# Kernel tuning notes

Hardware: AMD Instinct MI355X
Metric: run time of the kernel (lower is better)

The kernel has to match this reference:

```python
import jax, jax.numpy as jnp
import numpy as np

EPS = 1e-6
H = 12  # num_attention_heads

def _phi(x):
    # feature map used by fast-transformers LinearAttention: elu(x) + 1
    return jax.nn.elu(x) + 1.0

def setup_inputs() -> dict:
    key = jax.random.key(0)
    k1, k2, k3 = jax.random.split(key, 3)
    B, N, D = 32, 1024, 768
    x = jax.random.normal(k1, (B, N, D), dtype=jnp.float32)
    W_qkv = jax.random.normal(k2, (D, 3 * D), dtype=jnp.float32) * (D ** -0.5)
    W_out = jax.random.normal(k3, (D, D), dtype=jnp.float32) * (D ** -0.5)
    b_out = jnp.zeros((D,), dtype=jnp.float32)
    return {"x": x, "W_qkv": W_qkv, "W_out": W_out, "b_out": b_out}

def reference(x, W_qkv, W_out, b_out):
    B, N, D = x.shape
    d = D // H
    # F.pad(x, [0,0,0,1]): append one zero token along sequence
    x_ = jnp.pad(x, ((0, 0), (0, 1), (0, 0)))              # [B, N+1, D]
    qkv = x_ @ W_qkv                                        # [B, N+1, 3D]
    q, k, v = jnp.split(qkv, 3, axis=-1)
    q = q.reshape(B, N + 1, H, d)
    k = k.reshape(B, N + 1, H, d)
    v = v.reshape(B, N + 1, H, d)
    # non-causal linear attention (mask is all-ones -> no masking)
    q = _phi(q)
    k = _phi(k)
    kv = jnp.einsum('bshd,bshm->bhdm', k, v)                # [B, H, d, d]
    z = 1.0 / (jnp.einsum('blhd,bhd->blh', q, k.sum(axis=1)) + EPS)
    out = jnp.einsum('blhd,bhdm,blh->blhm', q, kv, z)       # [B, N+1, H, d]
    out = out.reshape(B, N + 1, D)
    out = out @ W_out + b_out                               # dropout = identity (eval)
    return out[:, :-1, :]                                   # drop padding token
```

## Files before the change

### kernel.cpp

```cpp
#include <hip/hip_runtime.h>
#include <hip/hip_bf16.h>


typedef __bf16 bf16x8 __attribute__((ext_vector_type(8)));
typedef float f32x4 __attribute__((ext_vector_type(4)));

__device__ __forceinline__ ushort f2bf(float f) {
  union { float f; unsigned u; } x; x.f = f;
  unsigned r = x.u + 0x7fffu + ((x.u >> 16) & 1u);
  return (ushort)(r >> 16);
}
__device__ __forceinline__ float bf2f(ushort h) {
  union { unsigned u; float f; } x; x.u = ((unsigned)h) << 16;
  return x.f;
}
__device__ __forceinline__ float bits2f(unsigned u) {
  union { unsigned u; float f; } x; x.u = u;
  return x.f;
}
__device__ __forceinline__ void gload_lds16(const void* g, void* lds) {
  __builtin_amdgcn_global_load_lds((const __attribute__((address_space(1))) void*)g,
                                   (__attribute__((address_space(3))) void*)lds, 16, 0, 0);
}

__global__ __launch_bounds__(256) void cvt_f32_bf16(const float* __restrict__ in,
                                                    ushort* __restrict__ out, int n4) {
  int i = blockIdx.x * 256 + threadIdx.x;
  if (i >= n4) return;
  float4 v = reinterpret_cast<const float4*>(in)[i];
  ushort4 o;
  o.x = f2bf(v.x); o.y = f2bf(v.y); o.z = f2bf(v.z); o.w = f2bf(v.w);
  reinterpret_cast<ushort4*>(out)[i] = o;
}

__global__ __launch_bounds__(256) void transpose_cvt(const float* __restrict__ src,
                                                     ushort* __restrict__ dst, int R, int C) {
  __shared__ float tile[32][33];
  int bc = blockIdx.x * 32, br = blockIdx.y * 32;
  int tx = threadIdx.x & 31, ty = threadIdx.x >> 5;
  #pragma unroll
  for (int i = 0; i < 32; i += 8)
    tile[ty + i][tx] = src[(size_t)(br + ty + i) * C + (bc + tx)];
  __syncthreads();
  #pragma unroll
  for (int i = 0; i < 32; i += 8)
    dst[(size_t)(bc + ty + i) * R + (br + tx)] = f2bf(tile[tx][ty + i]);
}

template <int MODE>
__global__ __launch_bounds__(512, 4) void gemm3b(const ushort* __restrict__ A,
                                                 const ushort* __restrict__ Bt,
                                                 void* __restrict__ C,
                                                 const float* __restrict__ bias,
                                                 int N, int K, int nbx, int cpx) {
  extern __shared__ ushort lds[];
  const int tid = threadIdx.x;
  const int lane = tid & 63;
  const int wid = tid >> 6;
  const int wm = wid >> 2, wn = wid & 3;
  const int laneR = lane & 15, laneS = lane >> 4;

  const int bid = blockIdx.x;
  const int lin = (bid & 7) * cpx + (bid >> 3);
  const int by = lin / nbx, bx = lin - by * nbx;
  const int m0 = by * 128, n0 = bx * 256;
  const int NT = K >> 5;

  const int sr = tid >> 2, ss = tid & 3;
  const int sslot = ss ^ ((sr >> 1) & 3);
  const ushort* Asrc = A + (size_t)(m0 + sr) * K + sslot * 8;
  const ushort* Bsrc = Bt + (size_t)(n0 + sr) * K + sslot * 8;
  const size_t rowstep128 = (size_t)128 * K;
  const int ldstA = tid * 8;
  const int ldstB = 4096 + tid * 8;

  const int sprime = laneS ^ ((laneR >> 1) & 3);
  const int aoff = (wm * 64 + laneR) * 32 + sprime * 8;
  const int boff = 4096 + (wn * 64 + laneR) * 32 + sprime * 8;

  f32x4 acc[4][4] = {};

  #define SBAR  __builtin_amdgcn_sched_barrier(0)
  #define STAGE_T(KT, DB)                                                         \
    { gload_lds16(Asrc + (KT) * 32, lds + (DB) + ldstA);                          \
      gload_lds16(Bsrc + (KT) * 32, lds + (DB) + ldstB);                          \
      gload_lds16(Bsrc + (KT) * 32 + rowstep128, lds + (DB) + ldstB + 4096); }

  STAGE_T(0, 0);
  STAGE_T(1, 12288);
  asm volatile("s_waitcnt vmcnt(3)" ::: "memory");
  SBAR;
  __builtin_amdgcn_s_barrier();
  SBAR;

  for (int t = 0; t < NT; ++t) {
    const ushort* cb = lds + (t % 3) * 12288;
    const int db2 = ((t + 2) % 3) * 12288;
    const int t2 = (t + 2 < NT) ? t + 2 : t;
    bf16x8 a[4], b[4];
    #pragma unroll
    for (int j = 0; j < 4; ++j) b[j] = *(const bf16x8*)(cb + boff + j * 512);
    #pragma unroll
    for (int i = 0; i < 4; ++i) a[i] = *(const bf16x8*)(cb + aoff + i * 512);
    STAGE_T(t2, db2);
    asm volatile("s_waitcnt vmcnt(3)" ::: "memory");
    SBAR;
    __builtin_amdgcn_s_barrier();
    SBAR;
    __builtin_amdgcn_s_setprio(1);
    #pragma unroll
    for (int i = 0; i < 4; ++i)
      #pragma unroll
      for (int j = 0; j < 4; ++j)
        acc[i][j] = __builtin_amdgcn_mfma_f32_16x16x32_bf16(a[i], b[j], acc[i][j], 0, 0, 0);
    __builtin_amdgcn_s_setprio(0);
    SBAR;
    __builtin_amdgcn_s_barrier();
    SBAR;
  }
  #undef STAGE_T
  asm volatile("s_waitcnt vmcnt(0)" ::: "memory");

  #pragma unroll
  for (int i = 0; i < 4; ++i) {
    const int grow0 = m0 + wm * 64 + i * 16 + (laneS << 2);
    #pragma unroll
    for (int j = 0; j < 4; ++j) {
      const int gcol = n0 + wn * 64 + j * 16 + laneR;
      #pragma unroll
      for (int r = 0; r < 4; ++r) {
        float v = acc[i][j][r];
        if (MODE == 0) {
          if (gcol < 1536) v = (v > 0.f) ? (v + 1.f) : __expf(v);
          reinterpret_cast<ushort*>(C)[(size_t)(grow0 + r) * N + gcol] = f2bf(v);
        } else {
          reinterpret_cast<float*>(C)[(size_t)(grow0 + r) * N + gcol] = v + bias[gcol];
        }
      }
    }
  }
}

__global__ __launch_bounds__(256) void kv_partial(const ushort* __restrict__ qkv,
                                                  float* __restrict__ kv_part,
                                                  float* __restrict__ ks_part) {
  const int blk = blockIdx.x;
  const int bh = blk >> 2, sp = blk & 3;
  const int b = bh / 12, h = bh % 12;
  const int tid = threadIdx.x;
  __shared__ float Ks[32 * 68];
  __shared__ float Vs[32 * 68];
  float acc[4][4] = {};
  float kacc[4] = {};
  const int dq0 = (tid & 15) * 4, mq0 = (tid >> 4) * 4;
  const int r = tid >> 3, o = (tid & 7) * 8;
  for (int st = 0; st < 256; st += 32) {
    const size_t rowbase = (size_t)(b * 1024 + sp * 256 + st + r) * 2304 + h * 64 + o;
    int4 kraw = *reinterpret_cast<const int4*>(qkv + rowbase + 768);
    int4 vraw = *reinterpret_cast<const int4*>(qkv + rowbase + 1536);
    float kf[8], vf[8];
    {
      const unsigned* kw = reinterpret_cast<const unsigned*>(&kraw);
      const unsigned* vw = reinterpret_cast<const unsigned*>(&vraw);
      #pragma unroll
      for (int w = 0; w < 4; ++w) {
        kf[2 * w]     = bits2f(kw[w] << 16);
        kf[2 * w + 1] = bits2f(kw[w] & 0xffff0000u);
        vf[2 * w]     = bits2f(vw[w] << 16);
        vf[2 * w + 1] = bits2f(vw[w] & 0xffff0000u);
      }
    }
    __syncthreads();
    #pragma unroll
    for (int w = 0; w < 8; ++w) {
      Ks[r * 68 + o + w] = kf[w];
      Vs[r * 68 + o + w] = vf[w];
    }
    __syncthreads();
    #pragma unroll 8
    for (int s = 0; s < 32; ++s) {
      f32x4 kk = *reinterpret_cast<const f32x4*>(&Ks[s * 68 + dq0]);
      f32x4 vv = *reinterpret_cast<const f32x4*>(&Vs[s * 68 + mq0]);
      #pragma unroll
      for (int jm = 0; jm < 4; ++jm)
        #pragma unroll
        for (int id = 0; id < 4; ++id)
          acc[jm][id] += vv[jm] * kk[id];
      if (mq0 == 0) {
        #pragma unroll
        for (int id = 0; id < 4; ++id) kacc[id] += kk[id];
      }
    }
  }
  float* kvp = kv_part + ((size_t)sp * 384 + bh) * 4096;
  #pragma unroll
  for (int jm = 0; jm < 4; ++jm)
    #pragma unroll
    for (int id = 0; id < 4; ++id)
      kvp[(mq0 + jm) * 64 + dq0 + id] = acc[jm][id];
  if (mq0 == 0) {
    #pragma unroll
    for (int id = 0; id < 4; ++id)
      ks_part[((size_t)sp * 384 + bh) * 64 + dq0 + id] = kacc[id];
  }
}

__global__ __launch_bounds__(256) void kv_reduce(const float* __restrict__ kv_part,
                                                 const float* __restrict__ ks_part,
                                                 ushort* __restrict__ kv_bf,
                                                 float* __restrict__ ksum) {
  int i = blockIdx.x * 256 + threadIdx.x;
  if (i < 384 * 4096) {
    float s = 0.f;
    #pragma unroll
    for (int p = 0; p < 4; ++p) s += kv_part[(size_t)p * (384 * 4096) + i];
    kv_bf[i] = f2bf(s);
  }
  if (i < 384 * 64) {
    float s = 1.0f;
    #pragma unroll
    for (int p = 0; p < 4; ++p) s += ks_part[(size_t)p * (384 * 64) + i];
    ksum[i] = s;
  }
}

__global__ __launch_bounds__(256) void attn_kernel(const ushort* __restrict__ qkv,
                                                   const ushort* __restrict__ kv_bf,
                                                   const float* __restrict__ ksum,
                                                   ushort* __restrict__ attn) {
  const int blk = blockIdx.x;
  const int bh = blk >> 3, tb = blk & 7;
  const int b = bh / 12, h = bh % 12;
  const int row0 = b * 1024 + tb * 128;
  __shared__ ushort Qs[128 * 64];
  __shared__ ushort KVs[64 * 64];
  __shared__ float zs[128];
  __shared__ float ks_lds[64];
  const int tid = threadIdx.x;
  const int lane = tid & 63, w = tid >> 6;
  #pragma unroll
  for (int j = 0; j < 4; ++j) {
    int c = j * 256 + tid;
    int qr = c >> 3, dsl = c & 7;
    int ssl = dsl ^ (qr & 7);
    gload_lds16(qkv + (size_t)(row0 + qr) * 2304 + h * 64 + ssl * 8, &Qs[c * 8]);
  }
  #pragma unroll
  for (int j = 0; j < 2; ++j) {
    int c = j * 256 + tid;
    int mr = c >> 3, dsl = c & 7;
    int ssl = dsl ^ (mr & 7);
    gload_lds16(kv_bf + (size_t)bh * 4096 + mr * 64 + ssl * 8, &KVs[c * 8]);
  }
  if (tid < 64) ks_lds[tid] = ksum[bh * 64 + tid];
  asm volatile("s_waitcnt vmcnt(0)" ::: "memory");
  __syncthreads();
  if (tid < 128) {
    float d = 0.f;
    const int tx7 = tid & 7;
    #pragma unroll
    for (int s = 0; s < 8; ++s) {
      int4 raw = *reinterpret_cast<const int4*>(&Qs[tid * 64 + ((s ^ tx7) << 3)]);
      const unsigned* wds = reinterpret_cast<const unsigned*>(&raw);
      #pragma unroll
      for (int w2 = 0; w2 < 4; ++w2) {
        d += bits2f(wds[w2] << 16) * ks_lds[s * 8 + 2 * w2];
        d += bits2f(wds[w2] & 0xffff0000u) * ks_lds[s * 8 + 2 * w2 + 1];
      }
    }
    zs[tid] = 1.f / (d + 1e-6f);
  }
  __syncthreads();
  f32x4 acc[2][4] = {};
  const int lr7 = (lane & 15) & 7;
  #pragma unroll
  for (int ks = 0; ks < 2; ++ks) {
    const int sxor = ((ks * 4 + (lane >> 4)) ^ lr7) << 3;
    bf16x8 a[2], bb[4];
    #pragma unroll
    for (int i = 0; i < 2; ++i)
      a[i] = *reinterpret_cast<const bf16x8*>(&Qs[(w * 32 + i * 16 + (lane & 15)) * 64 + sxor]);
    #pragma unroll
    for (int j = 0; j < 4; ++j)
      bb[j] = *reinterpret_cast<const bf16x8*>(&KVs[(j * 16 + (lane & 15)) * 64 + sxor]);
    #pragma unroll
    for (int i = 0; i < 2; ++i)
      #pragma unroll
      for (int j = 0; j < 4; ++j)
        acc[i][j] = __builtin_amdgcn_mfma_f32_16x16x32_bf16(a[i], bb[j], acc[i][j], 0, 0, 0);
  }
  #pragma unroll
  for (int i = 0; i < 2; ++i) {
    const int t0 = w * 32 + i * 16 + ((lane >> 4) << 2);
    #pragma unroll
    for (int j = 0; j < 4; ++j) {
      const int m = j * 16 + (lane & 15);
      #pragma unroll
      for (int r = 0; r < 4; ++r) {
        float v = acc[i][j][r] * zs[t0 + r];
        attn[(size_t)(row0 + t0 + r) * 768 + h * 64 + m] = f2bf(v);
      }
    }
  }
}

extern "C" void kernel_launch(void* const* d_in, const int* in_sizes, int n_in,
                              void* d_out, int out_size, void* d_ws, size_t ws_size,
                              hipStream_t stream) {
  (void)in_sizes; (void)n_in; (void)out_size; (void)ws_size;
  const float* x    = (const float*)d_in[0];
  const float* Wqkv = (const float*)d_in[1];
  const float* Wout = (const float*)d_in[2];
  const float* bout = (const float*)d_in[3];
  float* out = (float*)d_out;
  char* ws = (char*)d_ws;

  ushort* xbf    = (ushort*)(ws);
  ushort* wqkvT  = (ushort*)(ws + 50331648);
  ushort* woutT  = (ushort*)(ws + 53870592);
  ushort* qkv    = (ushort*)(ws + 55050240);
  float*  ksp    = (float*) (ws + 206045184);
  ushort* kvbf   = (ushort*)(ws + 206438400);
  float*  ksum   = (float*) (ws + 209584128);
  float*  kvpart = (float*)(ws);
  ushort* attn   = (ushort*)(ws);

  static const int LDS3 = 73728;
  hipFuncSetAttribute(reinterpret_cast<const void*>(&gemm3b<0>),
                      hipFuncAttributeMaxDynamicSharedMemorySize, LDS3);
  hipFuncSetAttribute(reinterpret_cast<const void*>(&gemm3b<1>),
                      hipFuncAttributeMaxDynamicSharedMemorySize, LDS3);

  cvt_f32_bf16<<<24576, 256, 0, stream>>>(x, xbf, 6291456);
  transpose_cvt<<<dim3(72, 24), 256, 0, stream>>>(Wqkv, wqkvT, 768, 2304);
  transpose_cvt<<<dim3(24, 24), 256, 0, stream>>>(Wout, woutT, 768, 768);
  gemm3b<0><<<2304, 512, LDS3, stream>>>(xbf, wqkvT, qkv, nullptr, 2304, 768, 9, 288);
  kv_partial<<<1536, 256, 0, stream>>>(qkv, kvpart, ksp);
  kv_reduce<<<6144, 256, 0, stream>>>(kvpart, ksp, kvbf, ksum);
  attn_kernel<<<3072, 256, 0, stream>>>(qkv, kvbf, ksum, attn);
  gemm3b<1><<<768, 512, LDS3, stream>>>(attn, woutT, out, bout, 768, 768, 3, 96);
}
```

Before: 290.4 us.

## Fuse fp32-to-bf16 conversion of x into the QKV GEMM prologue

```diff
diff --git a/kernel.cpp b/kernel.cpp
--- a/kernel.cpp
+++ b/kernel.cpp
@@ -4,6 +4,8 @@
 
 typedef __bf16 bf16x8 __attribute__((ext_vector_type(8)));
 typedef float f32x4 __attribute__((ext_vector_type(4)));
+
+#define SBAR  __builtin_amdgcn_sched_barrier(0)
 
 __device__ __forceinline__ ushort f2bf(float f) {
   union { float f; unsigned u; } x; x.f = f;
@@ -22,15 +24,23 @@
   __builtin_amdgcn_global_load_lds((const __attribute__((address_space(1))) void*)g,
                                    (__attribute__((address_space(3))) void*)lds, 16, 0, 0);
 }
-
-__global__ __launch_bounds__(256) void cvt_f32_bf16(const float* __restrict__ in,
-                                                    ushort* __restrict__ out, int n4) {
-  int i = blockIdx.x * 256 + threadIdx.x;
-  if (i >= n4) return;
-  float4 v = reinterpret_cast<const float4*>(in)[i];
-  ushort4 o;
-  o.x = f2bf(v.x); o.y = f2bf(v.y); o.z = f2bf(v.z); o.w = f2bf(v.w);
-  reinterpret_cast<ushort4*>(out)[i] = o;
+__device__ __forceinline__ void ds_write128(ushort* p, bf16x8 v) {
+  asm volatile("ds_write_b128 %0, %1"
+               :: "v"((__attribute__((address_space(3))) ushort*)p), "v"(v)
+               : "memory");
+}
+__device__ __forceinline__ f32x4 gloadf4(const float* p) {
+  f32x4 r;
+  asm volatile("global_load_dwordx4 %0, %1, off"
+               : "=v"(r)
+               : "v"(p));
+  return r;
+}
+__device__ __forceinline__ bf16x8 cvt8(f32x4 a, f32x4 b) {
+  bf16x8 v;
+  v[0] = (__bf16)a[0]; v[1] = (__bf16)a[1]; v[2] = (__bf16)a[2]; v[3] = (__bf16)a[3];
+  v[4] = (__bf16)b[0]; v[5] = (__bf16)b[1]; v[6] = (__bf16)b[2]; v[7] = (__bf16)b[3];
+  return v;
 }
 
 __global__ __launch_bounds__(256) void transpose_cvt(const float* __restrict__ src,
@@ -45,6 +55,115 @@
   #pragma unroll
   for (int i = 0; i < 32; i += 8)
     dst[(size_t)(bc + ty + i) * R + (br + tx)] = f2bf(tile[tx][ty + i]);
+}
+
+__global__ __launch_bounds__(512, 4) void gemm1f(const float* __restrict__ X,
+                                                 const ushort* __restrict__ Bt,
+                                                 ushort* __restrict__ C,
+                                                 int N, int K, int nbx, int cpx) {
+  extern __shared__ ushort lds[];
+  const int tid = threadIdx.x;
+  const int lane = tid & 63;
+  const int wid = tid >> 6;
+  const int wm = wid >> 2, wn = wid & 3;
+  const int laneR = lane & 15, laneS = lane >> 4;
+
+  const int bid = blockIdx.x;
+  const int lin = (bid & 7) * cpx + (bid >> 3);
+  const int by = lin / nbx, bx = lin - by * nbx;
+  const int m0 = by * 128, n0 = bx * 256;
+  const int NT = K >> 5;
+
+  const int sr = tid >> 2, ss = tid & 3;
+  const int sslot = ss ^ ((sr >> 1) & 3);
+  const float*  Axf  = X + (size_t)(m0 + sr) * K + sslot * 8;
+  const ushort* Bsrc = Bt + (size_t)(n0 + sr) * K + sslot * 8;
+  const size_t rowstep128 = (size_t)128 * K;
+  const int ldstA = tid * 8;
+  const int ldstB = 4096 + tid * 8;
+
+  const int sprime = laneS ^ ((laneR >> 1) & 3);
+  const int aoff = (wm * 64 + laneR) * 32 + sprime * 8;
+  const int boff = 4096 + (wn * 64 + laneR) * 32 + sprime * 8;
+
+  f32x4 acc[4][4] = {};
+  f32x4 rE0, rE1, rO0, rO1;
+
+  {
+    rE0 = gloadf4(Axf);      rE1 = gloadf4(Axf + 4);
+    rO0 = gloadf4(Axf + 32); rO1 = gloadf4(Axf + 36);
+    asm volatile("s_waitcnt vmcnt(0)" ::: "memory");
+    SBAR;
+    ds_write128(lds + ldstA, cvt8(rE0, rE1));
+    ds_write128(lds + 12288 + ldstA, cvt8(rO0, rO1));
+    gload_lds16(Bsrc,               lds + ldstB);
+    gload_lds16(Bsrc + rowstep128,  lds + ldstB + 4096);
+    gload_lds16(Bsrc + 32,              lds + 12288 + ldstB);
+    gload_lds16(Bsrc + 32 + rowstep128, lds + 12288 + ldstB + 4096);
+    rE0 = gloadf4(Axf + 64); rE1 = gloadf4(Axf + 68);
+    asm volatile("s_waitcnt vmcnt(0)" ::: "memory");
+    SBAR;
+    asm volatile("s_waitcnt lgkmcnt(0)" ::: "memory");
+    SBAR;
+    __builtin_amdgcn_s_barrier();
+    SBAR;
+  }
+
+  #define PHASE1F(T, WR0, WR1, IS0, IS1)                                          \
+  {                                                                               \
+    const int t_ = (T);                                                           \
+    const ushort* cb = lds + (t_ % 3) * 12288;                                    \
+    const int db2 = ((t_ + 2) % 3) * 12288;                                       \
+    const int t2 = (t_ + 2 < NT) ? t_ + 2 : t_;                                   \
+    const int t3 = (t_ + 3 < NT) ? t_ + 3 : t_;                                   \
+    bf16x8 a_[4], b_[4];                                                          \
+    _Pragma("unroll")                                                             \
+    for (int j = 0; j < 4; ++j) b_[j] = *(const bf16x8*)(cb + boff + j * 512);    \
+    _Pragma("unroll")                                                             \
+    for (int i = 0; i < 4; ++i) a_[i] = *(const bf16x8*)(cb + aoff + i * 512);    \
+    IS0 = gloadf4(Axf + t3 * 32); IS1 = gloadf4(Axf + t3 * 32 + 4);               \
+    gload_lds16(Bsrc + t2 * 32,              lds + db2 + ldstB);                  \
+    gload_lds16(Bsrc + t2 * 32 + rowstep128, lds + db2 + ldstB + 4096);           \
+    asm volatile("s_waitcnt vmcnt(4)" ::: "memory");                              \
+    SBAR;          \
+    ds_write128(lds + db2 + ldstA, cvt8(WR0, WR1));                               \
+    asm volatile("s_waitcnt lgkmcnt(0)" ::: "memory");                            \
+    SBAR;                                                                         \
+    __builtin_amdgcn_s_barrier();                                                 \
+    SBAR;                                                                         \
+    __builtin_amdgcn_s_setprio(1);                                                \
+    _Pragma("unroll")                                                             \
+    for (int i = 0; i < 4; ++i)                                                   \
+      _Pragma("unroll")                                                           \
+      for (int j = 0; j < 4; ++j)                                                 \
+        acc[i][j] = __builtin_amdgcn_mfma_f32_16x16x32_bf16(a_[i], b_[j], acc[i][j], 0, 0, 0); \
+    __builtin_amdgcn_s_setprio(0);                                                \
+    SBAR;                                                                         \
+    __builtin_amdgcn_s_barrier();                                                 \
+    SBAR;                                                                         \
+  }
+
+  for (int it = 0; it < NT; it += 2) {
+    PHASE1F(it,     rE0, rE1, rO0, rO1);
+    PHASE1F(it + 1, rO0, rO1, rE0, rE1);
+  }
+  #undef PHASE1F
+  asm volatile("s_waitcnt vmcnt(0)" ::: "memory");
+
+  #pragma unroll
+  for (int i = 0; i < 4; ++i) {
+    const int grow0 = m0 + wm * 64 + i * 16 + (laneS << 2);
+    #pragma unroll
+    for (int j = 0; j < 4; ++j) {
+      const int gcol = n0 + wn * 64 + j * 16 + laneR;
+      #pragma unroll
+      for (int r = 0; r < 4; ++r) {
+        float v = acc[i][j][r];
+        if (gcol < 1536) v = (v > 0.f) ? (v + 1.f) : __expf(v);
+        C[(size_t)(grow0 + r) * N + gcol] = f2bf(v);
+      }
+    }
+  }
 }
 
 template <int MODE>
@@ -80,7 +199,6 @@
 
   f32x4 acc[4][4] = {};
 
-  #define SBAR  __builtin_amdgcn_sched_barrier(0)
   #define STAGE_T(KT, DB)                                                         \
     { gload_lds16(Asrc + (KT) * 32, lds + (DB) + ldstA);                          \
       gload_lds16(Bsrc + (KT) * 32, lds + (DB) + ldstB);                          \
@@ -315,7 +433,6 @@
   float* out = (float*)d_out;
   char* ws = (char*)d_ws;
 
-  ushort* xbf    = (ushort*)(ws);
   ushort* wqkvT  = (ushort*)(ws + 50331648);
   ushort* woutT  = (ushort*)(ws + 53870592);
   ushort* qkv    = (ushort*)(ws + 55050240);
@@ -326,15 +443,14 @@
   ushort* attn   = (ushort*)(ws);
 
   static const int LDS3 = 73728;
-  hipFuncSetAttribute(reinterpret_cast<const void*>(&gemm3b<0>),
+  hipFuncSetAttribute(reinterpret_cast<const void*>(&gemm1f),
                       hipFuncAttributeMaxDynamicSharedMemorySize, LDS3);
   hipFuncSetAttribute(reinterpret_cast<const void*>(&gemm3b<1>),
                       hipFuncAttributeMaxDynamicSharedMemorySize, LDS3);
 
-  cvt_f32_bf16<<<24576, 256, 0, stream>>>(x, xbf, 6291456);
   transpose_cvt<<<dim3(72, 24), 256, 0, stream>>>(Wqkv, wqkvT, 768, 2304);
   transpose_cvt<<<dim3(24, 24), 256, 0, stream>>>(Wout, woutT, 768, 768);
-  gemm3b<0><<<2304, 512, LDS3, stream>>>(xbf, wqkvT, qkv, nullptr, 2304, 768, 9, 288);
+  gemm1f<<<2304, 512, LDS3, stream>>>(x, wqkvT, qkv, 2304, 768, 9, 288);
   kv_partial<<<1536, 256, 0, stream>>>(qkv, kvpart, ksp);
   kv_reduce<<<6144, 256, 0, stream>>>(kvpart, ksp, kvbf, ksum);
   attn_kernel<<<3072, 256, 0, stream>>>(qkv, kvbf, ksum, attn);
```

Result: slower. 345.2 us (+18.9%).

## Add 256x128-tile 4-wave QKV GEMM with fused elu+1 epilogue

Applied to the files above, without the earlier changes.

```diff
diff --git a/kernel.cpp b/kernel.cpp
--- a/kernel.cpp
+++ b/kernel.cpp
@@ -4,6 +4,8 @@
 
 typedef __bf16 bf16x8 __attribute__((ext_vector_type(8)));
 typedef float f32x4 __attribute__((ext_vector_type(4)));
+
+#define SBAR  __builtin_amdgcn_sched_barrier(0)
 
 __device__ __forceinline__ ushort f2bf(float f) {
   union { float f; unsigned u; } x; x.f = f;
@@ -45,6 +47,96 @@
   #pragma unroll
   for (int i = 0; i < 32; i += 8)
     dst[(size_t)(bc + ty + i) * R + (br + tx)] = f2bf(tile[tx][ty + i]);
+}
+
+__global__ __launch_bounds__(256, 2) void gemm1w(const ushort* __restrict__ A,
+                                                 const ushort* __restrict__ Bt,
+                                                 ushort* __restrict__ C,
+                                                 int N, int K, int nbx, int cpx) {
+  extern __shared__ ushort lds[];
+  const int tid = threadIdx.x;
+  const int lane = tid & 63;
+  const int wid = tid >> 6;
+  const int wm = wid >> 1, wn = wid & 1;
+  const int laneR = lane & 15, laneS = lane >> 4;
+
+  const int bid = blockIdx.x;
+  const int lin = (bid & 7) * cpx + (bid >> 3);
+  const int by = lin / nbx, bx = lin - by * nbx;
+  const int m0 = by * 256, n0 = bx * 128;
+  const int NT = K >> 5;
+
+  const int sr = tid >> 2, ss = tid & 3;
+  const int sslot = ss ^ ((sr >> 1) & 3);
+  const ushort* Asrc = A + (size_t)(m0 + sr) * K + sslot * 8;
+  const ushort* Bsrc = Bt + (size_t)(n0 + sr) * K + sslot * 8;
+  const size_t rowstep64 = (size_t)64 * K;
+  const int ldstA = tid * 8;
+  const int ldstB = 8192 + tid * 8;
+
+  const int sprime = laneS ^ ((laneR >> 1) & 3);
+  const int aoff = (wm * 128 + laneR) * 32 + sprime * 8;
+  const int boff = 8192 + (wn * 64 + laneR) * 32 + sprime * 8;
+
+  f32x4 acc[8][4] = {};
+
+  #define STAGE_T(KT, DB)                                                         \
+    { _Pragma("unroll")                                                           \
+      for (int k_ = 0; k_ < 4; ++k_)                                              \
+        gload_lds16(Asrc + (KT) * 32 + k_ * rowstep64, lds + (DB) + k_ * 2048 + ldstA); \
+      _Pragma("unroll")                                                           \
+      for (int k_ = 0; k_ < 2; ++k_)                                              \
+        gload_lds16(Bsrc + (KT) * 32 + k_ * rowstep64, lds + (DB) + k_ * 2048 + ldstB); }
+
+  STAGE_T(0, 0);
+  STAGE_T(1, 12288);
+  asm volatile("s_waitcnt vmcnt(6)" ::: "memory");
+  SBAR;
+  __builtin_amdgcn_s_barrier();
+  SBAR;
+
+  for (int t = 0; t < NT; ++t) {
+    const ushort* cb = lds + (t % 3) * 12288;
+    const int db2 = ((t + 2) % 3) * 12288;
+    const int t2 = (t + 2 < NT) ? t + 2 : t;
+    bf16x8 a[8], b[4];
+    #pragma unroll
+    for (int j = 0; j < 4; ++j) b[j] = *(const bf16x8*)(cb + boff + j * 512);
+    #pragma unroll
+    for (int i = 0; i < 8; ++i) a[i] = *(const bf16x8*)(cb + aoff + i * 512);
+    STAGE_T(t2, db2);
+    asm volatile("s_waitcnt vmcnt(6)" ::: "memory");
+    SBAR;
+    __builtin_amdgcn_s_barrier();
+    SBAR;
+    __builtin_amdgcn_s_setprio(1);
+    #pragma unroll
+    for (int i = 0; i < 8; ++i)
+      #pragma unroll
+      for (int j = 0; j < 4; ++j)
+        acc[i][j] = __builtin_amdgcn_mfma_f32_16x16x32_bf16(a[i], b[j], acc[i][j], 0, 0, 0);
+    __builtin_amdgcn_s_setprio(0);
+    SBAR;
+    __builtin_amdgcn_s_barrier();
+    SBAR;
+  }
+  #undef STAGE_T
+  asm volatile("s_waitcnt vmcnt(0)" ::: "memory");
+
+  #pragma unroll
+  for (int i = 0; i < 8; ++i) {
+    const int grow0 = m0 + wm * 128 + i * 16 + (laneS << 2);
+    #pragma unroll
+    for (int j = 0; j < 4; ++j) {
+      const int gcol = n0 + wn * 64 + j * 16 + laneR;
+      #pragma unroll
+      for (int r = 0; r < 4; ++r) {
+        float v = acc[i][j][r];
+        if (gcol < 1536) v = (v > 0.f) ? (v + 1.f) : __expf(v);
+        C[(size_t)(grow0 + r) * N + gcol] = f2bf(v);
+      }
+    }
+  }
 }
 
 template <int MODE>
@@ -80,7 +172,6 @@
 
   f32x4 acc[4][4] = {};
 
-  #define SBAR  __builtin_amdgcn_sched_barrier(0)
   #define STAGE_T(KT, DB)                                                         \
     { gload_lds16(Asrc + (KT) * 32, lds + (DB) + ldstA);                          \
       gload_lds16(Bsrc + (KT) * 32, lds + (DB) + ldstB);                          \
@@ -326,7 +417,7 @@
   ushort* attn   = (ushort*)(ws);
 
   static const int LDS3 = 73728;
-  hipFuncSetAttribute(reinterpret_cast<const void*>(&gemm3b<0>),
+  hipFuncSetAttribute(reinterpret_cast<const void*>(&gemm1w),
                       hipFuncAttributeMaxDynamicSharedMemorySize, LDS3);
   hipFuncSetAttribute(reinterpret_cast<const void*>(&gemm3b<1>),
                       hipFuncAttributeMaxDynamicSharedMemorySize, LDS3);
@@ -334,7 +425,7 @@
   cvt_f32_bf16<<<24576, 256, 0, stream>>>(x, xbf, 6291456);
   transpose_cvt<<<dim3(72, 24), 256, 0, stream>>>(Wqkv, wqkvT, 768, 2304);
   transpose_cvt<<<dim3(24, 24), 256, 0, stream>>>(Wout, woutT, 768, 768);
-  gemm3b<0><<<2304, 512, LDS3, stream>>>(xbf, wqkvT, qkv, nullptr, 2304, 768, 9, 288);
+  gemm1w<<<2304, 256, LDS3, stream>>>(xbf, wqkvT, qkv, 2304, 768, 18, 288);
   kv_partial<<<1536, 256, 0, stream>>>(qkv, kvpart, ksp);
   kv_reduce<<<6144, 256, 0, stream>>>(kvpart, ksp, kvbf, ksum);
   attn_kernel<<<3072, 256, 0, stream>>>(qkv, kvbf, ksum, attn);
```

After: 295.4 us. About the same (+1.7%).
